# Performance work log

Hardware: AMD Instinct MI355X
Metric: run time of the kernel (lower is better)

## Reference

```python
import jax, jax.numpy as jnp
import numpy as np

TEMPERATURE = 0.1


def setup_inputs() -> dict:
    key = jax.random.key(0)
    k1, k2 = jax.random.split(key)
    pred = jax.random.normal(k1, (4, 64, 32), dtype=jnp.float32)
    target = jax.random.normal(k2, (4, 64, 32), dtype=jnp.float32)
    return {"pred": pred, "target": target}


def reference(pred, target):
    # All inputs are finite and no mask is given, so valid_both is all-True and
    # the torch boolean flatten pred[valid_both] is exactly a reshape(-1).
    p = pred.reshape(-1)
    t = target.reshape(-1)
    n = p.shape[0]  # 8192
    # diff[i, j] = x[j] - x[i]; product is symmetric so orientation is irrelevant.
    pd = p[None, :] - p[:, None]           # [n, n]
    td = t[None, :] - t[:, None]           # [n, n]
    agreement = jnp.tanh(pd * td / TEMPERATURE)
    # mean over strict upper triangle (i < j): mask-and-sum, divide by pair count.
    upper = jnp.triu(jnp.ones((n, n), dtype=agreement.dtype), k=1)
    n_pairs = jnp.asarray(n * (n - 1) // 2, dtype=agreement.dtype)
    tau = jnp.sum(agreement * upper) / n_pairs
    return tau
```

## Files before the change

kernel.cpp:

```cpp
#include <hip/hip_runtime.h>


#define NTOT 8192
#define TPB  512
#define KPT  (NTOT / TPB)
#define JBLK 8
#define NBLK (NTOT / JBLK)

__global__ __launch_bounds__(TPB) void ktau_partial(const float* __restrict__ pred,
                                                    const float* __restrict__ targ,
                                                    double* __restrict__ partial) {
    const float C = 28.853900817779268f;
    const int tid = threadIdx.x;
    const int j0  = blockIdx.x * JBLK;

    float pj[JBLK], tj[JBLK];
#pragma unroll
    for (int jj = 0; jj < JBLK; ++jj) {
        pj[jj] = pred[j0 + jj];
        tj[jj] = targ[j0 + jj] * C;
    }

    float pi[KPT], ti[KPT];
#pragma unroll
    for (int k = 0; k < KPT; ++k) {
        const int i = tid + k * TPB;
        pi[k] = pred[i];
        ti[k] = targ[i] * C;
    }

    float acc[JBLK];
#pragma unroll
    for (int jj = 0; jj < JBLK; ++jj) acc[jj] = 0.0f;

#pragma unroll 2
    for (int k = 0; k < KPT; ++k) {
#pragma unroll
        for (int jj = 0; jj < JBLK; ++jj) {
            const float x = (pi[k] - pj[jj]) * (ti[k] - tj[jj]);
            const float e = __builtin_amdgcn_exp2f(x);
            const float r = __builtin_amdgcn_rcpf(e + 1.0f);
            acc[jj] = __builtin_fmaf(-2.0f, r, acc[jj]);
        }
    }

    float fsum = 0.0f;
#pragma unroll
    for (int jj = 0; jj < JBLK; ++jj) fsum += acc[jj];

    double dacc = (double)fsum;
#pragma unroll
    for (int off = 32; off > 0; off >>= 1)
        dacc += __shfl_down(dacc, off, 64);

    __shared__ double red[TPB / 64];
    const int wave = tid >> 6;
    if ((tid & 63) == 0) red[wave] = dacc;
    __syncthreads();
    if (tid == 0) {
        double s = 0.0;
#pragma unroll
        for (int w = 0; w < TPB / 64; ++w) s += red[w];
        partial[blockIdx.x] = s + (double)(TPB * KPT * JBLK);
    }
}

__global__ __launch_bounds__(256) void ktau_final(const double* __restrict__ partial,
                                                  float* __restrict__ out) {
    const int tid = threadIdx.x;
    double s = partial[tid] + partial[tid + 256] + partial[tid + 512] + partial[tid + 768];
#pragma unroll
    for (int off = 32; off > 0; off >>= 1)
        s += __shfl_down(s, off, 64);
    __shared__ double red[4];
    if ((tid & 63) == 0) red[tid >> 6] = s;
    __syncthreads();
    if (tid == 0) {
        const double t = red[0] + red[1] + red[2] + red[3];
        out[0] = (float)(t / ((double)NTOT * (double)(NTOT - 1)));
    }
}

extern "C" void kernel_launch(void* const* d_in, const int* in_sizes, int n_in,
                              void* d_out, int out_size, void* d_ws, size_t ws_size,
                              hipStream_t stream) {
    const float* pred = (const float*)d_in[0];
    const float* targ = (const float*)d_in[1];
    float* out = (float*)d_out;
    double* partial = (double*)d_ws;

    ktau_partial<<<NBLK, TPB, 0, stream>>>(pred, targ, partial);
    ktau_final<<<1, 256, 0, stream>>>(partial, out);
}
```

Baseline: 71.44 us.

## Fuse final reduction via atomic counter, replace rcp with Newton iterations

Merges the two-kernel reduction into one kernel: the last block to finish, detected with an atomic counter, reduces all partials and writes the output. A memset resets the counter before each launch. The per-pair hardware reciprocal is replaced by a bit-trick initial guess refined by three Newton steps, with the exp2 argument clamped to keep the guess in range. It also switches the i-operand loads to float4 and raises the inner unroll factor. The reciprocal change trades one transcendental instruction for several full-rate ALU ops per pair, which may add work in the hot loop.

```diff
diff --git a/kernel.cpp b/kernel.cpp
--- a/kernel.cpp
+++ b/kernel.cpp
@@ -7,12 +7,15 @@
 #define JBLK 8
 #define NBLK (NTOT / JBLK)
 
-__global__ __launch_bounds__(TPB) void ktau_partial(const float* __restrict__ pred,
-                                                    const float* __restrict__ targ,
-                                                    double* __restrict__ partial) {
+__global__ __launch_bounds__(TPB) void ktau_fused(const float* __restrict__ pred,
+                                                  const float* __restrict__ targ,
+                                                  double* __restrict__ partial,
+                                                  unsigned* __restrict__ counter,
+                                                  float* __restrict__ out) {
     const float C = 28.853900817779268f;
     const int tid = threadIdx.x;
-    const int j0  = blockIdx.x * JBLK;
+    const int bid = blockIdx.x;
+    const int j0  = bid * JBLK;
 
     float pj[JBLK], tj[JBLK];
 #pragma unroll
@@ -22,24 +25,32 @@
     }
 
     float pi[KPT], ti[KPT];
+    const float4* p4 = (const float4*)pred;
+    const float4* t4 = (const float4*)targ;
 #pragma unroll
-    for (int k = 0; k < KPT; ++k) {
-        const int i = tid + k * TPB;
-        pi[k] = pred[i];
-        ti[k] = targ[i] * C;
+    for (int q = 0; q < KPT / 4; ++q) {
+        const float4 a = p4[tid + q * TPB];
+        const float4 b = t4[tid + q * TPB];
+        pi[4*q+0] = a.x; pi[4*q+1] = a.y; pi[4*q+2] = a.z; pi[4*q+3] = a.w;
+        ti[4*q+0] = b.x * C; ti[4*q+1] = b.y * C; ti[4*q+2] = b.z * C; ti[4*q+3] = b.w * C;
     }
 
     float acc[JBLK];
 #pragma unroll
     for (int jj = 0; jj < JBLK; ++jj) acc[jj] = 0.0f;
 
-#pragma unroll 2
+#pragma unroll 4
     for (int k = 0; k < KPT; ++k) {
 #pragma unroll
         for (int jj = 0; jj < JBLK; ++jj) {
-            const float x = (pi[k] - pj[jj]) * (ti[k] - tj[jj]);
+            float x = (pi[k] - pj[jj]) * (ti[k] - tj[jj]);
+            x = __builtin_amdgcn_fmed3f(x, -28.0f, 28.0f);
             const float e = __builtin_amdgcn_exp2f(x);
-            const float r = __builtin_amdgcn_rcpf(e + 1.0f);
+            const float d = e + 1.0f;
+            float r = __uint_as_float(0x7EF311C3u - __float_as_uint(d));
+            r = r * __builtin_fmaf(-d, r, 2.0f);
+            r = r * __builtin_fmaf(-d, r, 2.0f);
+            r = r * __builtin_fmaf(-d, r, 2.0f);
             acc[jj] = __builtin_fmaf(-2.0f, r, acc[jj]);
         }
     }
@@ -54,30 +65,35 @@
         dacc += __shfl_down(dacc, off, 64);
 
     __shared__ double red[TPB / 64];
-    const int wave = tid >> 6;
-    if ((tid & 63) == 0) red[wave] = dacc;
+    __shared__ int s_last;
+    if ((tid & 63) == 0) red[tid >> 6] = dacc;
     __syncthreads();
     if (tid == 0) {
         double s = 0.0;
 #pragma unroll
         for (int w = 0; w < TPB / 64; ++w) s += red[w];
-        partial[blockIdx.x] = s + (double)(TPB * KPT * JBLK);
+        partial[bid] = s + (double)(TPB * KPT * JBLK);
+        __threadfence();
+        const unsigned old = atomicAdd(counter, 1u);
+        s_last = (old == NBLK - 1) ? 1 : 0;
     }
-}
+    __syncthreads();
 
-__global__ __launch_bounds__(256) void ktau_final(const double* __restrict__ partial,
-                                                  float* __restrict__ out) {
-    const int tid = threadIdx.x;
-    double s = partial[tid] + partial[tid + 256] + partial[tid + 512] + partial[tid + 768];
+    if (s_last) {
+        __threadfence();
+        double s = partial[tid] + partial[tid + TPB];
 #pragma unroll
-    for (int off = 32; off > 0; off >>= 1)
-        s += __shfl_down(s, off, 64);
-    __shared__ double red[4];
-    if ((tid & 63) == 0) red[tid >> 6] = s;
-    __syncthreads();
-    if (tid == 0) {
-        const double t = red[0] + red[1] + red[2] + red[3];
-        out[0] = (float)(t / ((double)NTOT * (double)(NTOT - 1)));
+        for (int off = 32; off > 0; off >>= 1)
+            s += __shfl_down(s, off, 64);
+        __shared__ double red2[TPB / 64];
+        if ((tid & 63) == 0) red2[tid >> 6] = s;
+        __syncthreads();
+        if (tid == 0) {
+            double t = 0.0;
+#pragma unroll
+            for (int w = 0; w < TPB / 64; ++w) t += red2[w];
+            out[0] = (float)(t / ((double)NTOT * (double)(NTOT - 1)));
+        }
     }
 }
 
@@ -88,7 +104,8 @@
     const float* targ = (const float*)d_in[1];
     float* out = (float*)d_out;
     double* partial = (double*)d_ws;
+    unsigned* counter = (unsigned*)((char*)d_ws + NBLK * sizeof(double));
 
-    ktau_partial<<<NBLK, TPB, 0, stream>>>(pred, targ, partial);
-    ktau_final<<<1, 256, 0, stream>>>(partial, out);
+    hipMemsetAsync(counter, 0, sizeof(unsigned), stream);
+    ktau_fused<<<NBLK, TPB, 0, stream>>>(pred, targ, partial, counter, out);
 }
```

Result: slower. 86.86 us (+21.6%).
